# Kernel tuning notes

Measured on AMD Instinct MI355X. Metric: run time of the kernel, lower is better.

Reference implementation:

```python
import jax, jax.numpy as jnp
import numpy as np

N, E1, E2, P, H = 4096, 131072, 131072, 65536, 128
ROLE_VOCAB, ROLE_DIM, IDX_VOCAB, IDX_DIM = 8, 16, 1024, 8


def _lin_init(key, fan_in, fan_out):
    k1, k2 = jax.random.split(key)
    bound = 1.0 / np.sqrt(fan_in)
    W = jax.random.uniform(k1, (fan_in, fan_out), jnp.float32, -bound, bound)
    b = jax.random.uniform(k2, (fan_out,), jnp.float32, -bound, bound)
    return W, b


def setup_inputs() -> dict:
    key = jax.random.key(0)
    ks = jax.random.split(key, 24)
    d = {}
    d["block_features"] = jax.random.normal(ks[0], (N, 16), jnp.float32)
    d["role_ids"] = jax.random.randint(ks[1], (N,), 0, ROLE_VOCAB)
    d["b2b_src"] = jax.random.randint(ks[2], (E1,), 0, N)
    d["b2b_dst"] = jax.random.randint(ks[3], (E1,), 0, N)
    d["b2b_w"] = jax.random.uniform(ks[4], (E1,), jnp.float32)
    d["p2b_pin"] = jax.random.randint(ks[5], (E2,), 0, P)
    d["p2b_block"] = jax.random.randint(ks[6], (E2,), 0, N)
    d["p2b_w"] = jax.random.uniform(ks[7], (E2,), jnp.float32)
    d["pins_pos"] = jax.random.normal(ks[8], (P, 2), jnp.float32)
    d["area_targets"] = jax.random.uniform(ks[9], (N,), jnp.float32)
    # parameters
    d["role_emb"] = jax.random.normal(ks[10], (ROLE_VOCAB, ROLE_DIM), jnp.float32)
    d["idx_emb"] = jax.random.normal(ks[11], (IDX_VOCAB, IDX_DIM), jnp.float32)
    d["in_W1"], d["in_b1"] = _lin_init(ks[12], 16 + IDX_DIM + ROLE_DIM, H)
    d["in_W2"], d["in_b2"] = _lin_init(ks[13], H, H)
    d["b2b_W1"], d["b2b_b1"] = _lin_init(ks[14], 2 * H + 1, H)
    d["b2b_W2"], d["b2b_b2"] = _lin_init(ks[15], H, H)
    d["p2b_W1"], d["p2b_b1"] = _lin_init(ks[16], H + 3, H)
    d["p2b_W2"], d["p2b_b2"] = _lin_init(ks[17], H, H)
    d["self_W"], d["self_b"] = _lin_init(ks[18], H, H)
    d["ln_g"] = jnp.ones((H,), jnp.float32)
    d["ln_b"] = jnp.zeros((H,), jnp.float32)
    d["gp_W1"], d["gp_b1"] = _lin_init(ks[19], 2 * H, H)
    d["gp_W2"], d["gp_b2"] = _lin_init(ks[20], H, H)
    return d


def _mlp2(x, W1, b1, W2, b2):
    return jax.nn.relu(x @ W1 + b1) @ W2 + b2


def _forward(block_features, role_ids, b2b_src, b2b_dst, b2b_w, p2b_pin, p2b_block,
             p2b_w, pins_pos, area_targets, role_emb, idx_emb, in_W1, in_b1, in_W2,
             in_b2, b2b_W1, b2b_b1, b2b_W2, b2b_b2, p2b_W1, p2b_b1, p2b_W2, p2b_b2,
             self_W, self_b, ln_g, ln_b, gp_W1, gp_b1, gp_W2, gp_b2):
    n = block_features.shape[0]
    role_e = role_emb[role_ids]                       # [N, role_dim]
    idx_e = idx_emb[jnp.arange(n) % IDX_VOCAB]        # [N, idx_dim]
    x = jnp.concatenate([block_features, role_e, idx_e], axis=-1)
    h = jax.nn.relu(_mlp2(x, in_W1, in_b1, in_W2, in_b2))  # input_proj ends in ReLU

    # --- b2b messages: two directed messages per undirected edge ---
    max_b2b = jax.lax.stop_gradient(jnp.maximum(jnp.max(jnp.abs(b2b_w)), 1.0))
    w = (b2b_w / max_b2b)[:, None]                    # [E1, 1]
    hi, hj = h[b2b_src], h[b2b_dst]                   # [E1, H]
    m_ij = _mlp2(jnp.concatenate([hi, hj, w], -1), b2b_W1, b2b_b1, b2b_W2, b2b_b2)
    m_ji = _mlp2(jnp.concatenate([hj, hi, w], -1), b2b_W1, b2b_b1, b2b_W2, b2b_b2)
    agg = jnp.zeros_like(h).at[b2b_src].add(m_ij).at[b2b_dst].add(m_ji)

    # --- p2b messages ---
    total_area = jnp.maximum(jnp.sum(area_targets), 1e-6)
    case_scale = jax.lax.stop_gradient(jnp.maximum(jnp.sqrt(total_area), 1e-6))
    max_p2b = jax.lax.stop_gradient(jnp.maximum(jnp.max(jnp.abs(p2b_w)), 1.0))
    pin_feats = jnp.concatenate(
        [pins_pos[p2b_pin] / case_scale, (p2b_w / max_p2b)[:, None]], axis=-1)  # [E2, 3]
    m_p = _mlp2(jnp.concatenate([h[p2b_block], pin_feats], -1),
                p2b_W1, p2b_b1, p2b_W2, p2b_b2)
    agg = agg.at[p2b_block].add(m_p)

    # --- combine + LayerNorm ---
    z = h @ self_W + self_b + agg
    mu = jnp.mean(z, axis=-1, keepdims=True)
    var = jnp.mean(jnp.square(z - mu), axis=-1, keepdims=True)
    block_embeddings = (z - mu) / jnp.sqrt(var + 1e-5) * ln_g + ln_b

    pooled = jnp.concatenate(
        [block_embeddings.mean(axis=0), block_embeddings.max(axis=0)], axis=-1)
    graph_embedding = _mlp2(pooled, gp_W1, gp_b1, gp_W2, gp_b2)
    return block_embeddings, graph_embedding


def reference(block_features, role_ids, b2b_src, b2b_dst, b2b_w, p2b_pin, p2b_block,
              p2b_w, pins_pos, area_targets, role_emb, idx_emb, in_W1, in_b1, in_W2,
              in_b2, b2b_W1, b2b_b1, b2b_W2, b2b_b2, p2b_W1, p2b_b1, p2b_W2, p2b_b2,
              self_W, self_b, ln_g, ln_b, gp_W1, gp_b1, gp_W2, gp_b2):
    block_embeddings, graph_embedding = _forward(
        block_features, role_ids, b2b_src, b2b_dst, b2b_w, p2b_pin, p2b_block,
        p2b_w, pins_pos, area_targets, role_emb, idx_emb, in_W1, in_b1, in_W2,
        in_b2, b2b_W1, b2b_b1, b2b_W2, b2b_b2, p2b_W1, p2b_b1, p2b_W2, p2b_b2,
        self_W, self_b, ln_g, ln_b, gp_W1, gp_b1, gp_W2, gp_b2)
    block_mask = jnp.ones((block_features.shape[0],), dtype=bool)
    return block_embeddings, graph_embedding, block_mask
```

## Files before the change

kernel.cpp:

```cpp
#include <hip/hip_runtime.h>
#include <hip/hip_bf16.h>

#define N_NODES 4096
#define HDIM    128
#define E1      131072
#define E2      131072
#define NMSG_B2B (2 * E1)
#define CAPB    192
#define CAPP    96

#define OFF_PSUM   8
#define OFF_PMAX   136
#define OFF_HB     264
#define OFF_P      (OFF_HB + 262144)
#define OFF_Q      (OFF_P + 524288)
#define OFF_R      (OFF_Q + 524288)
#define OFF_CP     (OFF_R + 524288)
#define OFF_B2H    (OFF_CP + 24576)
#define OFF_B2L    (OFF_B2H + 8192)
#define OFF_P2H    (OFF_B2L + 8192)
#define OFF_P2L    (OFF_P2H + 8192)
#define OFF_SWP    (OFF_P2L + 8192)
#define OFF_IW1    (OFF_SWP + 8192)
#define OFF_IW2    (OFF_IW1 + 4096)
#define OFF_WLAST  (OFF_IW2 + 8192)
#define OFF_PEXTRA (OFF_WLAST + 128)
#define OFF_CNTB   (OFF_PEXTRA + 384)
#define OFF_CNTP   (OFF_CNTB + 4096)
#define OFF_BKB    (OFF_CNTP + 4096)
#define OFF_BKP    (OFF_BKB + 2 * N_NODES * CAPB)
#define WS_FLOATS  (OFF_BKP + 2 * N_NODES * CAPP)

typedef short short8 __attribute__((ext_vector_type(8)));
typedef float f32x4 __attribute__((ext_vector_type(4)));

__device__ __forceinline__ unsigned short f2bf(float f) {
  union { float f; unsigned u; } v; v.f = f;
  unsigned r = v.u + 0x7fffu + ((v.u >> 16) & 1u);
  return (unsigned short)(r >> 16);
}
__device__ __forceinline__ float bf2f(unsigned short h) {
  return __uint_as_float((unsigned)h << 16);
}
__device__ __forceinline__ int il(int c) { return ((c & 63) << 1) | (c >> 6); }

__global__ __launch_bounds__(256) void setup_kernel(const float* __restrict__ b2bw,
                                                    const float* __restrict__ p2bw,
                                                    const float* __restrict__ area,
                                                    const float* __restrict__ bW1,
                                                    const float* __restrict__ bW2,
                                                    const float* __restrict__ pW1,
                                                    const float* __restrict__ pW2,
                                                    const float* __restrict__ sWm,
                                                    const float* __restrict__ iW1,
                                                    const float* __restrict__ iW2,
                                                    float* __restrict__ ws) {
  __shared__ float red[256];
  int b = blockIdx.x, t = threadIdx.x;
  if (b < 32) {
    float m = 0.f;
    for (int i = b * 256 + t; i < E1; i += 32 * 256) m = fmaxf(m, fabsf(b2bw[i]));
    red[t] = m; __syncthreads();
    for (int s = 128; s > 0; s >>= 1) { if (t < s) red[t] = fmaxf(red[t], red[t + s]); __syncthreads(); }
    if (t == 0) atomicMax((unsigned*)&ws[0], __float_as_uint(red[0]));
  } else if (b < 64) {
    float m = 0.f;
    for (int i = (b - 32) * 256 + t; i < E2; i += 32 * 256) m = fmaxf(m, fabsf(p2bw[i]));
    red[t] = m; __syncthreads();
    for (int s = 128; s > 0; s >>= 1) { if (t < s) red[t] = fmaxf(red[t], red[t + s]); __syncthreads(); }
    if (t == 0) atomicMax((unsigned*)&ws[1], __float_as_uint(red[0]));
  } else if (b < 96) {
    float s0 = 0.f;
    for (int i = (b - 64) * 256 + t; i < N_NODES; i += 32 * 256) s0 += area[i];
    red[t] = s0; __syncthreads();
    for (int s = 128; s > 0; s >>= 1) { if (t < s) red[t] += red[t + s]; __syncthreads(); }
    if (t == 0) atomicAdd(&ws[2], red[0]);
  } else if (b == 96) {
    if (t < HDIM) ((int*)ws)[OFF_PMAX + t] = 0x80000000;
  } else {
    unsigned short* Cp  = (unsigned short*)(ws + OFF_CP);
    unsigned short* B2h = (unsigned short*)(ws + OFF_B2H);
    unsigned short* B2l = (unsigned short*)(ws + OFF_B2L);
    unsigned short* P2h = (unsigned short*)(ws + OFF_P2H);
    unsigned short* P2l = (unsigned short*)(ws + OFF_P2L);
    unsigned short* Swp = (unsigned short*)(ws + OFF_SWP);
    unsigned short* I1p = (unsigned short*)(ws + OFF_IW1);
    unsigned short* I2p = (unsigned short*)(ws + OFF_IW2);
    float* wlast = ws + OFF_WLAST;
    float* pextra = ws + OFF_PEXTRA;
    const int total = 156160;
    for (int x = (b - 97) * 256 + t; x < total; x += 128 * 256) {
      if (x < 49152) {
        int j = x & 7, lane = (x >> 3) & 63, ks = (x >> 9) & 3, nc = x >> 11;
        int col = nc * 16 + (lane & 15), k = ks * 32 + (lane >> 4) * 8 + j;
        float v;
        if (col < 128)      v = bW1[k * 128 + col];
        else if (col < 256) v = bW1[(128 + k) * 128 + (col - 128)];
        else                v = pW1[k * 128 + (col - 256)];
        Cp[x] = f2bf(v);
      } else if (x < 114688) {
        int u = (x - 49152) & 16383, which = (x - 49152) >> 14;
        int j = u & 7, lane = (u >> 3) & 63, ks = (u >> 9) & 3, nt = u >> 11;
        int n = nt * 16 + (lane & 15), k = ks * 32 + (lane >> 4) * 8 + j;
        float v = (which < 2) ? bW2[k * 128 + n] : pW2[k * 128 + n];
        unsigned short hi = f2bf(v);
        unsigned short outv = (which & 1) ? f2bf(v - bf2f(hi)) : hi;
        ((which < 2) ? ((which & 1) ? B2l : B2h) : ((which & 1) ? P2l : P2h))[u] = outv;
      } else if (x < 131072) {
        int u = x - 114688;
        int j = u & 7, lane = (u >> 3) & 63, ks = (u >> 9) & 3, nt = u >> 11;
        int n = nt * 16 + (lane & 15), k = ks * 32 + (lane >> 4) * 8 + j;
        Swp[u] = f2bf(sWm[k * 128 + n]);
      } else if (x < 139264) {
        int u = x - 131072;
        int j = u & 7, lane = (u >> 3) & 63, ks = (u >> 9) & 1, nt = u >> 10;
        int n = nt * 16 + (lane & 15), k = ks * 32 + (lane >> 4) * 8 + j;
        I1p[u] = (k < 40) ? f2bf(iW1[k * 128 + n]) : 0;
      } else if (x < 155648) {
        int u = x - 139264;
        int j = u & 7, lane = (u >> 3) & 63, ks = (u >> 9) & 3, nt = u >> 11;
        int n = nt * 16 + (lane & 15), k = ks * 32 + (lane >> 4) * 8 + j;
        I2p[u] = f2bf(iW2[k * 128 + n]);
      } else if (x < 155776) {
        int c = x - 155648;
        wlast[il(c)] = bW1[256 * 128 + c];
      } else {
        int u = x - 155776;
        int r = u >> 7, c = u & 127;
        pextra[r * 128 + il(c)] = pW1[(128 + r) * 128 + c];
      }
    }
  }
}

__global__ __launch_bounds__(512) void mid_kernel(const int* __restrict__ src,
                                                  const int* __restrict__ dst,
                                                  const int* __restrict__ pblk,
                                                  const int* __restrict__ ppin,
                                                  const float* __restrict__ bwv,
                                                  const float* __restrict__ pwv,
                                                  const float* __restrict__ pins,
                                                  const float* __restrict__ bfeat,
                                                  const int* __restrict__ rid,
                                                  const float* __restrict__ remb,
                                                  const float* __restrict__ iemb,
                                                  const float* __restrict__ ib1,
                                                  const float* __restrict__ ib2,
                                                  const float* __restrict__ bb1,
                                                  const float* __restrict__ pb1,
                                                  float* __restrict__ ws,
                                                  unsigned short* __restrict__ hb) {
  __shared__ __attribute__((aligned(16))) unsigned short xs[16 * 72];
  __shared__ __attribute__((aligned(16))) unsigned short h1s[16 * 136];
  __shared__ __attribute__((aligned(16))) unsigned short hs[16 * 136];
  int tid = threadIdx.x;
  if (blockIdx.x < 768) {
    int i = blockIdx.x * 512 + tid;
    int* cntB = (int*)ws + OFF_CNTB;
    int* cntP = (int*)ws + OFF_CNTP;
    uint2* BKB = (uint2*)((int*)ws + OFF_BKB);
    uint2* BKP = (uint2*)((int*)ws + OFF_BKP);
    if (i < NMSG_B2B) {
      int e = i >> 1, d = i & 1;
      int tg = d ? dst[e] : src[e];
      int o  = d ? src[e] : dst[e];
      int pos = atomicAdd(&cntB[tg], 1);
      if (pos < CAPB) {
        uint2 v; v.x = (unsigned)o; v.y = __float_as_uint(bwv[e]);
        BKB[tg * CAPB + pos] = v;
      }
    } else {
      int e = i - NMSG_B2B;
      int pin = ppin[e];
      int tg = pblk[e];
      int pos = atomicAdd(&cntP[tg], 1);
      if (pos < CAPP) {
        uint2 v;
        v.x = ((unsigned)f2bf(pins[pin * 2 + 1]) << 16) | (unsigned)f2bf(pins[pin * 2]);
        v.y = __float_as_uint(pwv[e]);
        BKP[tg * CAPP + pos] = v;
      }
    }
    return;
  }
  const unsigned short* I1p = (const unsigned short*)(ws + OFF_IW1);
  const unsigned short* I2p = (const unsigned short*)(ws + OFF_IW2);
  const unsigned short* Cp  = (const unsigned short*)(ws + OFF_CP);
  float* P = ws + OFF_P;
  float* Q = ws + OFF_Q;
  float* R = ws + OFF_R;
  int n0 = (blockIdx.x - 768) * 16;
  for (int idx = tid; idx < 1024; idx += 512) {
    int m = idx >> 6, c = idx & 63;
    int n = n0 + m;
    float v = 0.f;
    if (c < 16)      v = bfeat[n * 16 + c];
    else if (c < 32) v = remb[rid[n] * 16 + (c - 16)];
    else if (c < 40) v = iemb[(n & 1023) * 8 + (c - 32)];
    xs[m * 72 + c] = f2bf(v);
  }
  __syncthreads();
  int lane = tid & 63, wv = tid >> 6;
  int l15 = lane & 15, q = lane >> 4;
  f32x4 zero = {0.f, 0.f, 0.f, 0.f};
  f32x4 a1 = zero;
#pragma unroll
  for (int ks = 0; ks < 2; ks++) {
    short8 af = *(const short8*)(&xs[l15 * 72 + ks * 32 + q * 8]);
    short8 bfr = *(const short8*)(I1p + ((wv * 2 + ks) * 64 + lane) * 8);
    a1 = __builtin_amdgcn_mfma_f32_16x16x32_bf16(af, bfr, a1, 0, 0, 0);
  }
  {
    int n = wv * 16 + l15;
    float b = ib1[n];
#pragma unroll
    for (int r = 0; r < 4; r++)
      h1s[(q * 4 + r) * 136 + n] = f2bf(fmaxf(a1[r] + b, 0.f));
  }
  __syncthreads();
  f32x4 a2 = zero;
#pragma unroll
  for (int ks = 0; ks < 4; ks++) {
    short8 af = *(const short8*)(&h1s[l15 * 136 + ks * 32 + q * 8]);
    short8 bfr = *(const short8*)(I2p + ((wv * 4 + ks) * 64 + lane) * 8);
    a2 = __builtin_amdgcn_mfma_f32_16x16x32_bf16(af, bfr, a2, 0, 0, 0);
  }
  {
    int n = wv * 16 + l15;
    float b = ib2[n];
#pragma unroll
    for (int r = 0; r < 4; r++) {
      unsigned short hv = f2bf(fmaxf(a2[r] + b, 0.f));
      hs[(q * 4 + r) * 136 + n] = hv;
      hb[(n0 + q * 4 + r) * 128 + n] = hv;
    }
  }
  __syncthreads();
  f32x4 a3[3];
#pragma unroll
  for (int i = 0; i < 3; i++) a3[i] = zero;
#pragma unroll
  for (int ks = 0; ks < 4; ks++) {
    short8 af = *(const short8*)(&hs[l15 * 136 + ks * 32 + q * 8]);
#pragma unroll
    for (int j = 0; j < 3; j++) {
      short8 bfr = *(const short8*)(Cp + (((3 * wv + j) * 4 + ks) * 64 + lane) * 8);
      a3[j] = __builtin_amdgcn_mfma_f32_16x16x32_bf16(af, bfr, a3[j], 0, 0, 0);
    }
  }
#pragma unroll
  for (int j = 0; j < 3; j++) {
    int col = (3 * wv + j) * 16 + l15;
    int arr = col >> 7, cc = col & 127;
    float bias = (arr == 0) ? bb1[cc] : ((arr == 2) ? pb1[cc] : 0.f);
    float* dstp = (arr == 0) ? P : ((arr == 1) ? Q : R);
    int ic = il(cc);
#pragma unroll
    for (int r = 0; r < 4; r++)
      dstp[(n0 + q * 4 + r) * 128 + ic] = a3[j][r] + bias;
  }
}

__global__ __launch_bounds__(1024) void fused_kernel(const unsigned short* __restrict__ hb,
                                                     const float* __restrict__ sb,
                                                     const float* __restrict__ lng,
                                                     const float* __restrict__ lnb,
                                                     const float* __restrict__ bb2,
                                                     const float* __restrict__ pb2,
                                                     const float* __restrict__ gW1,
                                                     const float* __restrict__ gb1,
                                                     const float* __restrict__ gW2,
                                                     const float* __restrict__ gb2,
                                                     float* __restrict__ ws,
                                                     float* __restrict__ out) {
  __shared__ __attribute__((aligned(16))) unsigned short A[16 * 648];
  __shared__ float zp[2][16 * 128];
  __shared__ float zs[16 * 133];
  __shared__ float muS[16], rsg[16];
  __shared__ float partS[16][16], partQ[16][16];
  __shared__ float psumL[8][128];
  __shared__ int   pmaxL[8][128];
  __shared__ int   isLast;
  int tid = threadIdx.x;
  int n0 = blockIdx.x * 16;
  int lane = tid & 63, wv = tid >> 6;
  if (tid < 256) {
    int m = tid >> 4, o = (tid & 15) * 8;
    *(uint4*)(&A[m * 648 + o]) = *(const uint4*)(hb + (n0 + m) * 128 + o);
  }
  {
    const int* cntB = (const int*)ws + OFF_CNTB;
    const int* cntP = (const int*)ws + OFF_CNTP;
    const uint2* BKB = (const uint2*)((const int*)ws + OFF_BKB);
    const uint2* BKP = (const uint2*)((const int*)ws + OFF_BKP);
    const float* Pm = ws + OFF_P;
    const float* Qm = ws + OFF_Q;
    const float* Rm = ws + OFF_R;
    float invb = 1.f / fmaxf(__uint_as_float(((const unsigned*)ws)[0]), 1.f);
    float invp = 1.f / fmaxf(__uint_as_float(((const unsigned*)ws)[1]), 1.f);
    float cs = fmaxf(sqrtf(fmaxf(ws[2], 1e-6f)), 1e-6f);
    float invc = 1.f / cs;
    float2 wlr = *(const float2*)(ws + OFF_WLAST + 2 * lane);
    float2 e0r = *(const float2*)(ws + OFF_PEXTRA + 2 * lane);
    float2 e1r = *(const float2*)(ws + OFF_PEXTRA + 128 + 2 * lane);
    float2 e2r = *(const float2*)(ws + OFF_PEXTRA + 256 + 2 * lane);
    float2 wl = {invb * wlr.x, invb * wlr.y};
    float2 e0 = {invc * e0r.x, invc * e0r.y};
    float2 e1 = {invc * e1r.x, invc * e1r.y};
    float2 e2 = {invp * e2r.x, invp * e2r.y};
    int ln = wv;
    int node = n0 + ln;
    {
      int cnt = min(cntB[node], CAPB);
      const uint2* bk = BKB + node * CAPB;
      float2 p = *(const float2*)(Pm + node * 128 + 2 * lane);
      float a0 = 0.f, a1 = 0.f, b0 = 0.f, b1 = 0.f;
      int m = 0;
      for (; m + 8 <= cnt; m += 8) {
        uint2 k0 = bk[m],     k1 = bk[m + 1], k2 = bk[m + 2], k3 = bk[m + 3];
        uint2 k4 = bk[m + 4], k5 = bk[m + 5], k6 = bk[m + 6], k7 = bk[m + 7];
        float2 q0 = *(const float2*)(Qm + k0.x * 128 + 2 * lane);
        float2 q1 = *(const float2*)(Qm + k1.x * 128 + 2 * lane);
        float2 q2 = *(const float2*)(Qm + k2.x * 128 + 2 * lane);
        float2 q3 = *(const float2*)(Qm + k3.x * 128 + 2 * lane);
        float2 q4 = *(const float2*)(Qm + k4.x * 128 + 2 * lane);
        float2 q5 = *(const float2*)(Qm + k5.x * 128 + 2 * lane);
        float2 q6 = *(const float2*)(Qm + k6.x * 128 + 2 * lane);
        float2 q7 = *(const float2*)(Qm + k7.x * 128 + 2 * lane);
        float w0 = __uint_as_float(k0.y), w1 = __uint_as_float(k1.y);
        float w2 = __uint_as_float(k2.y), w3 = __uint_as_float(k3.y);
        float w4 = __uint_as_float(k4.y), w5 = __uint_as_float(k5.y);
        float w6 = __uint_as_float(k6.y), w7 = __uint_as_float(k7.y);
        a0 += fmaxf(fmaf(w0, wl.x, p.x) + q0.x, 0.f);
        a1 += fmaxf(fmaf(w0, wl.y, p.y) + q0.y, 0.f);
        b0 += fmaxf(fmaf(w1, wl.x, p.x) + q1.x, 0.f);
        b1 += fmaxf(fmaf(w1, wl.y, p.y) + q1.y, 0.f);
        a0 += fmaxf(fmaf(w2, wl.x, p.x) + q2.x, 0.f);
        a1 += fmaxf(fmaf(w2, wl.y, p.y) + q2.y, 0.f);
        b0 += fmaxf(fmaf(w3, wl.x, p.x) + q3.x, 0.f);
        b1 += fmaxf(fmaf(w3, wl.y, p.y) + q3.y, 0.f);
        a0 += fmaxf(fmaf(w4, wl.x, p.x) + q4.x, 0.f);
        a1 += fmaxf(fmaf(w4, wl.y, p.y) + q4.y, 0.f);
        b0 += fmaxf(fmaf(w5, wl.x, p.x) + q5.x, 0.f);
        b1 += fmaxf(fmaf(w5, wl.y, p.y) + q5.y, 0.f);
        a0 += fmaxf(fmaf(w6, wl.x, p.x) + q6.x, 0.f);
        a1 += fmaxf(fmaf(w6, wl.y, p.y) + q6.y, 0.f);
        b0 += fmaxf(fmaf(w7, wl.x, p.x) + q7.x, 0.f);
        b1 += fmaxf(fmaf(w7, wl.y, p.y) + q7.y, 0.f);
      }
      for (; m < cnt; m++) {
        uint2 k0 = bk[m];
        float w0 = __uint_as_float(k0.y);
        float2 q0 = *(const float2*)(Qm + k0.x * 128 + 2 * lane);
        a0 += fmaxf(fmaf(w0, wl.x, p.x) + q0.x, 0.f);
        a1 += fmaxf(fmaf(w0, wl.y, p.y) + q0.y, 0.f);
      }
      float s0 = a0 + b0;
      float s1 = a1 + b1;
      unsigned short h0 = f2bf(s0);
      A[ln * 648 + 128 + lane] = h0;
      A[ln * 648 + 256 + lane] = f2bf(s0 - bf2f(h0));
      unsigned short h1v = f2bf(s1);
      A[ln * 648 + 128 + 64 + lane] = h1v;
      A[ln * 648 + 256 + 64 + lane] = f2bf(s1 - bf2f(h1v));
    }
    {
      int cnt = min(cntP[node], CAPP);
      const uint2* bk = BKP + node * CAPP;
      float2 r = *(const float2*)(Rm + node * 128 + 2 * lane);
      float a0 = 0.f, a1 = 0.f, b0 = 0.f, b1 = 0.f;
      int m = 0;
      for (; m + 4 <= cnt; m += 4) {
        uint2 k0 = bk[m], k1 = bk[m + 1], k2 = bk[m + 2], k3 = bk[m + 3];
        float x00 = __uint_as_float((k0.x & 0xFFFFu) << 16);
        float x01 = __uint_as_float(k0.x & 0xFFFF0000u);
        float x02 = __uint_as_float(k0.y);
        float x10 = __uint_as_float((k1.x & 0xFFFFu) << 16);
        float x11 = __uint_as_float(k1.x & 0xFFFF0000u);
        float x12 = __uint_as_float(k1.y);
        float x20 = __uint_as_float((k2.x & 0xFFFFu) << 16);
        float x21 = __uint_as_float(k2.x & 0xFFFF0000u);
        float x22 = __uint_as_float(k2.y);
        float x30 = __uint_as_float((k3.x & 0xFFFFu) << 16);
        float x31 = __uint_as_float(k3.x & 0xFFFF0000u);
        float x32 = __uint_as_float(k3.y);
        a0 += fmaxf(fmaf(x02, e2.x, fmaf(x01, e1.x, fmaf(x00, e0.x, r.x))), 0.f);
        a1 += fmaxf(fmaf(x02, e2.y, fmaf(x01, e1.y, fmaf(x00, e0.y, r.y))), 0.f);
        b0 += fmaxf(fmaf(x12, e2.x, fmaf(x11, e1.x, fmaf(x10, e0.x, r.x))), 0.f);
        b1 += fmaxf(fmaf(x12, e2.y, fmaf(x11, e1.y, fmaf(x10, e0.y, r.y))), 0.f);
        a0 += fmaxf(fmaf(x22, e2.x, fmaf(x21, e1.x, fmaf(x20, e0.x, r.x))), 0.f);
        a1 += fmaxf(fmaf(x22, e2.y, fmaf(x21, e1.y, fmaf(x20, e0.y, r.y))), 0.f);
        b0 += fmaxf(fmaf(x32, e2.x, fmaf(x31, e1.x, fmaf(x30, e0.x, r.x))), 0.f);
        b1 += fmaxf(fmaf(x32, e2.y, fmaf(x31, e1.y, fmaf(x30, e0.y, r.y))), 0.f);
      }
      for (; m < cnt; m++) {
        uint2 k0 = bk[m];
        float x00 = __uint_as_float((k0.x & 0xFFFFu) << 16);
        float x01 = __uint_as_float(k0.x & 0xFFFF0000u);
        float x02 = __uint_as_float(k0.y);
        a0 += fmaxf(fmaf(x02, e2.x, fmaf(x01, e1.x, fmaf(x00, e0.x, r.x))), 0.f);
        a1 += fmaxf(fmaf(x02, e2.y, fmaf(x01, e1.y, fmaf(x00, e0.y, r.y))), 0.f);
      }
      float s0 = a0 + b0;
      float s1 = a1 + b1;
      unsigned short h0 = f2bf(s0);
      A[ln * 648 + 384 + lane] = h0;
      A[ln * 648 + 512 + lane] = f2bf(s0 - bf2f(h0));
      unsigned short h1v = f2bf(s1);
      A[ln * 648 + 384 + 64 + lane] = h1v;
      A[ln * 648 + 512 + 64 + lane] = f2bf(s1 - bf2f(h1v));
    }
  }
  __syncthreads();
  int l15 = lane & 15, q = lane >> 4;
  int ct = wv & 7, half = wv >> 3;
  f32x4 zero = {0.f, 0.f, 0.f, 0.f};
  f32x4 acc = zero;
  const unsigned short* bufs[7] = {
    (const unsigned short*)(ws + OFF_SWP), (const unsigned short*)(ws + OFF_B2H),
    (const unsigned short*)(ws + OFF_B2L), (const unsigned short*)(ws + OFF_B2H),
    (const unsigned short*)(ws + OFF_P2H), (const unsigned short*)(ws + OFF_P2L),
    (const unsigned short*)(ws + OFF_P2H)};
  const int segs[7] = {0, 128, 128, 256, 384, 384, 512};
  int p0 = half ? 4 : 0, p1 = half ? 7 : 4;
  for (int p = p0; p < p1; p++) {
#pragma unroll
    for (int ks = 0; ks < 4; ks++) {
      short8 af = *(const short8*)(&A[l15 * 648 + segs[p] + ks * 32 + q * 8]);
      short8 bfr = *(const short8*)(bufs[p] + ((ct * 4 + ks) * 64 + lane) * 8);
      acc = __builtin_amdgcn_mfma_f32_16x16x32_bf16(af, bfr, acc, 0, 0, 0);
    }
  }
  {
    int nn = ct * 16 + l15;
#pragma unroll
    for (int r = 0; r < 4; r++)
      zp[half][(q * 4 + r) * 128 + nn] = acc[r];
  }
  __syncthreads();
  const int* cntB = (const int*)ws + OFF_CNTB;
  const int* cntP = (const int*)ws + OFF_CNTP;
  {
    int idx = tid;
    for (int rep = 0; rep < 2; rep++, idx += 1024) {
      int row = idx >> 7, c = idx & 127;
      float cb = (float)cntB[n0 + row], cp = (float)cntP[n0 + row];
      zs[row * 133 + c] = zp[0][row * 128 + c] + zp[1][row * 128 + c]
                        + sb[c] + cb * bb2[c] + cp * pb2[c];
    }
  }
  __syncthreads();
  if (tid < 256) {
    int r = tid >> 4, g = tid & 15;
    const float* zr = &zs[r * 133 + g * 8];
    float s = 0.f, s2 = 0.f;
#pragma unroll
    for (int i = 0; i < 8; i++) { float v = zr[i]; s += v; s2 += v * v; }
    partS[r][g] = s; partQ[r][g] = s2;
  }
  __syncthreads();
  if (tid < 16) {
    float s = 0.f, s2 = 0.f;
#pragma unroll
    for (int g = 0; g < 16; g++) { s += partS[tid][g]; s2 += partQ[tid][g]; }
    float m = s * (1.f / 128.f);
    float var = s2 * (1.f / 128.f) - m * m;
    muS[tid] = m;
    rsg[tid] = rsqrtf(fmaxf(var, 0.f) + 1e-5f);
  }
  __syncthreads();
  {
    int c = tid & 127, grp = tid >> 7;
    float g = lng[c], b = lnb[c];
    float ls = 0.f; int lm = 0x80000000;
    for (int r = grp * 2; r < grp * 2 + 2; r++) {
      float v = (zs[r * 133 + c] - muS[r]) * rsg[r] * g + b;
      out[(n0 + r) * 128 + c] = v;
      ls += v;
      int e = __float_as_int(v);
      e = e >= 0 ? e : (e ^ 0x7fffffff);
      lm = max(lm, e);
    }
    psumL[grp][c] = ls; pmaxL[grp][c] = lm;
  }
  __syncthreads();
  if (tid < 128) {
    float s = 0.f; int mx = 0x80000000;
#pragma unroll
    for (int g = 0; g < 8; g++) { s += psumL[g][tid]; mx = max(mx, pmaxL[g][tid]); }
    atomicAdd(&ws[OFF_PSUM + tid], s);
    atomicMax(&((int*)ws)[OFF_PMAX + tid], mx);
  }
  if (tid < 16) out[N_NODES * HDIM + HDIM + n0 + tid] = 1.0f;
  __syncthreads();
  if (tid == 0) {
    __threadfence();
    int v = atomicAdd(&((int*)ws)[3], 1);
    isLast = (v == (int)gridDim.x - 1);
  }
  __syncthreads();
  if (!isLast) return;
  __shared__ float pooled[256];
  __shared__ float gpart[8][128];
  __shared__ float g1[128];
  if (tid < 128) {
    pooled[tid] = atomicAdd(&ws[OFF_PSUM + tid], 0.f) * (1.f / (float)N_NODES);
  } else if (tid < 256) {
    int e = atomicAdd(&((int*)ws)[OFF_PMAX + (tid - 128)], 0);
    int bits = e >= 0 ? e : (e ^ 0x7fffffff);
    pooled[tid] = __int_as_float(bits);
  }
  __syncthreads();
  {
    int c = tid & 127, g = tid >> 7;
    float acc2 = 0.f;
#pragma unroll 8
    for (int k = g * 32; k < g * 32 + 32; k++) acc2 += pooled[k] * gW1[k * 128 + c];
    gpart[g][c] = acc2;
  }
  __syncthreads();
  if (tid < 128) {
    float s = gb1[tid];
#pragma unroll
    for (int g = 0; g < 8; g++) s += gpart[g][tid];
    g1[tid] = fmaxf(s, 0.f);
  }
  __syncthreads();
  {
    int c = tid & 127, g = tid >> 7;
    float acc2 = 0.f;
#pragma unroll 8
    for (int k = g * 16; k < g * 16 + 16; k++) acc2 += g1[k] * gW2[k * 128 + c];
    gpart[g][c] = acc2;
  }
  __syncthreads();
  if (tid < 128) {
    float s = gb2[tid];
#pragma unroll
    for (int g = 0; g < 8; g++) s += gpart[g][tid];
    out[N_NODES * HDIM + tid] = s;
  }
}

extern "C" void kernel_launch(void* const* d_in, const int* in_sizes, int n_in,
                              void* d_out, int out_size, void* d_ws, size_t ws_size,
                              hipStream_t stream) {
  const float* bfeat = (const float*)d_in[0];
  const int*   rid   = (const int*)d_in[1];
  const int*   bsrc  = (const int*)d_in[2];
  const int*   bdst  = (const int*)d_in[3];
  const float* bw    = (const float*)d_in[4];
  const int*   ppin  = (const int*)d_in[5];
  const int*   pblk  = (const int*)d_in[6];
  const float* pw    = (const float*)d_in[7];
  const float* pins  = (const float*)d_in[8];
  const float* area  = (const float*)d_in[9];
  const float* remb  = (const float*)d_in[10];
  const float* iemb  = (const float*)d_in[11];
  const float* inW1  = (const float*)d_in[12];
  const float* inb1  = (const float*)d_in[13];
  const float* inW2  = (const float*)d_in[14];
  const float* inb2  = (const float*)d_in[15];
  const float* bW1   = (const float*)d_in[16];
  const float* bb1   = (const float*)d_in[17];
  const float* bW2   = (const float*)d_in[18];
  const float* bb2   = (const float*)d_in[19];
  const float* pW1   = (const float*)d_in[20];
  const float* pb1   = (const float*)d_in[21];
  const float* pW2   = (const float*)d_in[22];
  const float* pb2   = (const float*)d_in[23];
  const float* sW    = (const float*)d_in[24];
  const float* sb    = (const float*)d_in[25];
  const float* lng   = (const float*)d_in[26];
  const float* lnb   = (const float*)d_in[27];
  const float* gW1   = (const float*)d_in[28];
  const float* gb1   = (const float*)d_in[29];
  const float* gW2   = (const float*)d_in[30];
  const float* gb2   = (const float*)d_in[31];

  float* ws  = (float*)d_ws;
  float* out = (float*)d_out;
  unsigned short* hb = (unsigned short*)(ws + OFF_HB);
  int* cntB = (int*)ws + OFF_CNTB;

  hipMemsetAsync(d_ws, 0, 264 * sizeof(float), stream);
  hipMemsetAsync((void*)cntB, 0, 2 * 4096 * sizeof(int), stream);
  setup_kernel<<<225, 256, 0, stream>>>(bw, pw, area,
                                        bW1, bW2, pW1, pW2, sW, inW1, inW2, ws);
  mid_kernel<<<1024, 512, 0, stream>>>(bsrc, bdst, pblk, ppin, bw, pw, pins,
                                       bfeat, rid, remb, iemb, inb1, inb2, bb1, pb1,
                                       ws, hb);
  fused_kernel<<<256, 1024, 0, stream>>>(hb, sb, lng, lnb, bb2, pb2,
                                         gW1, gb1, gW2, gb2, ws, out);
}
```

Measured before the change: 196.0 us.

## Move edge bucketing into setup kernel and widen node kernel to 1024 threads

```diff
diff --git a/kernel.cpp b/kernel.cpp
--- a/kernel.cpp
+++ b/kernel.cpp
@@ -47,6 +47,11 @@
 __global__ __launch_bounds__(256) void setup_kernel(const float* __restrict__ b2bw,
                                                     const float* __restrict__ p2bw,
                                                     const float* __restrict__ area,
+                                                    const int* __restrict__ src,
+                                                    const int* __restrict__ dst,
+                                                    const int* __restrict__ pblk,
+                                                    const int* __restrict__ ppin,
+                                                    const float* __restrict__ pins,
                                                     const float* __restrict__ bW1,
                                                     const float* __restrict__ bW2,
                                                     const float* __restrict__ pW1,
@@ -77,6 +82,33 @@
     if (t == 0) atomicAdd(&ws[2], red[0]);
   } else if (b == 96) {
     if (t < HDIM) ((int*)ws)[OFF_PMAX + t] = 0x80000000;
+  } else if (b < 1633) {
+    int i = (b - 97) * 256 + t;
+    int* cntB = (int*)ws + OFF_CNTB;
+    int* cntP = (int*)ws + OFF_CNTP;
+    uint2* BKB = (uint2*)((int*)ws + OFF_BKB);
+    uint2* BKP = (uint2*)((int*)ws + OFF_BKP);
+    if (i < NMSG_B2B) {
+      int e = i >> 1, d = i & 1;
+      int tg = d ? dst[e] : src[e];
+      int o  = d ? src[e] : dst[e];
+      int pos = atomicAdd(&cntB[tg], 1);
+      if (pos < CAPB) {
+        uint2 v; v.x = (unsigned)o; v.y = __float_as_uint(b2bw[e]);
+        BKB[tg * CAPB + pos] = v;
+      }
+    } else if (i < NMSG_B2B + E2) {
+      int e = i - NMSG_B2B;
+      int pin = ppin[e];
+      int tg = pblk[e];
+      int pos = atomicAdd(&cntP[tg], 1);
+      if (pos < CAPP) {
+        uint2 v;
+        v.x = ((unsigned)f2bf(pins[pin * 2 + 1]) << 16) | (unsigned)f2bf(pins[pin * 2]);
+        v.y = __float_as_uint(p2bw[e]);
+        BKP[tg * CAPP + pos] = v;
+      }
+    }
   } else {
     unsigned short* Cp  = (unsigned short*)(ws + OFF_CP);
     unsigned short* B2h = (unsigned short*)(ws + OFF_B2H);
@@ -89,7 +121,7 @@
     float* wlast = ws + OFF_WLAST;
     float* pextra = ws + OFF_PEXTRA;
     const int total = 156160;
-    for (int x = (b - 97) * 256 + t; x < total; x += 128 * 256) {
+    for (int x = (b - 1633) * 256 + t; x < total; x += 128 * 256) {
       if (x < 49152) {
         int j = x & 7, lane = (x >> 3) & 63, ks = (x >> 9) & 3, nc = x >> 11;
         int col = nc * 16 + (lane & 15), k = ks * 32 + (lane >> 4) * 8 + j;
@@ -133,65 +165,29 @@
   }
 }
 
-__global__ __launch_bounds__(512) void mid_kernel(const int* __restrict__ src,
-                                                  const int* __restrict__ dst,
-                                                  const int* __restrict__ pblk,
-                                                  const int* __restrict__ ppin,
-                                                  const float* __restrict__ bwv,
-                                                  const float* __restrict__ pwv,
-                                                  const float* __restrict__ pins,
-                                                  const float* __restrict__ bfeat,
-                                                  const int* __restrict__ rid,
-                                                  const float* __restrict__ remb,
-                                                  const float* __restrict__ iemb,
-                                                  const float* __restrict__ ib1,
-                                                  const float* __restrict__ ib2,
-                                                  const float* __restrict__ bb1,
-                                                  const float* __restrict__ pb1,
-                                                  float* __restrict__ ws,
-                                                  unsigned short* __restrict__ hb) {
+__global__ __launch_bounds__(1024) void node_kernel(const float* __restrict__ bfeat,
+                                                    const int* __restrict__ rid,
+                                                    const float* __restrict__ remb,
+                                                    const float* __restrict__ iemb,
+                                                    const float* __restrict__ ib1,
+                                                    const float* __restrict__ ib2,
+                                                    const float* __restrict__ bb1,
+                                                    const float* __restrict__ pb1,
+                                                    float* __restrict__ ws,
+                                                    unsigned short* __restrict__ hb) {
   __shared__ __attribute__((aligned(16))) unsigned short xs[16 * 72];
   __shared__ __attribute__((aligned(16))) unsigned short h1s[16 * 136];
   __shared__ __attribute__((aligned(16))) unsigned short hs[16 * 136];
   int tid = threadIdx.x;
-  if (blockIdx.x < 768) {
-    int i = blockIdx.x * 512 + tid;
-    int* cntB = (int*)ws + OFF_CNTB;
-    int* cntP = (int*)ws + OFF_CNTP;
-    uint2* BKB = (uint2*)((int*)ws + OFF_BKB);
-    uint2* BKP = (uint2*)((int*)ws + OFF_BKP);
-    if (i < NMSG_B2B) {
-      int e = i >> 1, d = i & 1;
-      int tg = d ? dst[e] : src[e];
-      int o  = d ? src[e] : dst[e];
-      int pos = atomicAdd(&cntB[tg], 1);
-      if (pos < CAPB) {
-        uint2 v; v.x = (unsigned)o; v.y = __float_as_uint(bwv[e]);
-        BKB[tg * CAPB + pos] = v;
-      }
-    } else {
-      int e = i - NMSG_B2B;
-      int pin = ppin[e];
-      int tg = pblk[e];
-      int pos = atomicAdd(&cntP[tg], 1);
-      if (pos < CAPP) {
-        uint2 v;
-        v.x = ((unsigned)f2bf(pins[pin * 2 + 1]) << 16) | (unsigned)f2bf(pins[pin * 2]);
-        v.y = __float_as_uint(pwv[e]);
-        BKP[tg * CAPP + pos] = v;
-      }
-    }
-    return;
-  }
   const unsigned short* I1p = (const unsigned short*)(ws + OFF_IW1);
   const unsigned short* I2p = (const unsigned short*)(ws + OFF_IW2);
   const unsigned short* Cp  = (const unsigned short*)(ws + OFF_CP);
   float* P = ws + OFF_P;
   float* Q = ws + OFF_Q;
   float* R = ws + OFF_R;
-  int n0 = (blockIdx.x - 768) * 16;
-  for (int idx = tid; idx < 1024; idx += 512) {
-    int m = idx >> 6, c = idx & 63;
+  int n0 = blockIdx.x * 16;
+  if (tid < 1024) {
+    int m = tid >> 6, c = tid & 63;
     int n = n0 + m;
     float v = 0.f;
     if (c < 16)      v = bfeat[n * 16 + c];
@@ -203,14 +199,14 @@
   int lane = tid & 63, wv = tid >> 6;
   int l15 = lane & 15, q = lane >> 4;
   f32x4 zero = {0.f, 0.f, 0.f, 0.f};
-  f32x4 a1 = zero;
-#pragma unroll
-  for (int ks = 0; ks < 2; ks++) {
-    short8 af = *(const short8*)(&xs[l15 * 72 + ks * 32 + q * 8]);
-    short8 bfr = *(const short8*)(I1p + ((wv * 2 + ks) * 64 + lane) * 8);
-    a1 = __builtin_amdgcn_mfma_f32_16x16x32_bf16(af, bfr, a1, 0, 0, 0);
-  }
-  {
+  if (wv < 8) {
+    f32x4 a1 = zero;
+#pragma unroll
+    for (int ks = 0; ks < 2; ks++) {
+      short8 af = *(const short8*)(&xs[l15 * 72 + ks * 32 + q * 8]);
+      short8 bfr = *(const short8*)(I1p + ((wv * 2 + ks) * 64 + lane) * 8);
+      a1 = __builtin_amdgcn_mfma_f32_16x16x32_bf16(af, bfr, a1, 0, 0, 0);
+    }
     int n = wv * 16 + l15;
     float b = ib1[n];
 #pragma unroll
@@ -218,14 +214,14 @@
       h1s[(q * 4 + r) * 136 + n] = f2bf(fmaxf(a1[r] + b, 0.f));
   }
   __syncthreads();
-  f32x4 a2 = zero;
-#pragma unroll
-  for (int ks = 0; ks < 4; ks++) {
-    short8 af = *(const short8*)(&h1s[l15 * 136 + ks * 32 + q * 8]);
-    short8 bfr = *(const short8*)(I2p + ((wv * 4 + ks) * 64 + lane) * 8);
-    a2 = __builtin_amdgcn_mfma_f32_16x16x32_bf16(af, bfr, a2, 0, 0, 0);
-  }
-  {
+  if (wv < 8) {
+    f32x4 a2 = zero;
+#pragma unroll
+    for (int ks = 0; ks < 4; ks++) {
+      short8 af = *(const short8*)(&h1s[l15 * 136 + ks * 32 + q * 8]);
+      short8 bfr = *(const short8*)(I2p + ((wv * 4 + ks) * 64 + lane) * 8);
+      a2 = __builtin_amdgcn_mfma_f32_16x16x32_bf16(af, bfr, a2, 0, 0, 0);
+    }
     int n = wv * 16 + l15;
     float b = ib2[n];
 #pragma unroll
@@ -236,21 +232,24 @@
     }
   }
   __syncthreads();
-  f32x4 a3[3];
-#pragma unroll
-  for (int i = 0; i < 3; i++) a3[i] = zero;
+  int tiles[2];
+  tiles[0] = wv;
+  tiles[1] = (wv < 8) ? (16 + wv) : -1;
+  f32x4 a3[2]; a3[0] = zero; a3[1] = zero;
 #pragma unroll
   for (int ks = 0; ks < 4; ks++) {
     short8 af = *(const short8*)(&hs[l15 * 136 + ks * 32 + q * 8]);
 #pragma unroll
-    for (int j = 0; j < 3; j++) {
-      short8 bfr = *(const short8*)(Cp + (((3 * wv + j) * 4 + ks) * 64 + lane) * 8);
+    for (int j = 0; j < 2; j++) {
+      if (tiles[j] < 0) continue;
+      short8 bfr = *(const short8*)(Cp + ((tiles[j] * 4 + ks) * 64 + lane) * 8);
       a3[j] = __builtin_amdgcn_mfma_f32_16x16x32_bf16(af, bfr, a3[j], 0, 0, 0);
     }
   }
 #pragma unroll
-  for (int j = 0; j < 3; j++) {
-    int col = (3 * wv + j) * 16 + l15;
+  for (int j = 0; j < 2; j++) {
+    if (tiles[j] < 0) continue;
+    int col = tiles[j] * 16 + l15;
     int arr = col >> 7, cc = col & 127;
     float bias = (arr == 0) ? bb1[cc] : ((arr == 2) ? pb1[cc] : 0.f);
     float* dstp = (arr == 0) ? P : ((arr == 1) ? Q : R);
@@ -511,7 +510,7 @@
     pooled[tid] = __int_as_float(bits);
   }
   __syncthreads();
-  {
+  if (tid < 1024) {
     int c = tid & 127, g = tid >> 7;
     float acc2 = 0.f;
 #pragma unroll 8
@@ -526,7 +525,7 @@
     g1[tid] = fmaxf(s, 0.f);
   }
   __syncthreads();
-  {
+  if (tid < 1024) {
     int c = tid & 127, g = tid >> 7;
     float acc2 = 0.f;
 #pragma unroll 8
@@ -585,11 +584,10 @@
 
   hipMemsetAsync(d_ws, 0, 264 * sizeof(float), stream);
   hipMemsetAsync((void*)cntB, 0, 2 * 4096 * sizeof(int), stream);
-  setup_kernel<<<225, 256, 0, stream>>>(bw, pw, area,
-                                        bW1, bW2, pW1, pW2, sW, inW1, inW2, ws);
-  mid_kernel<<<1024, 512, 0, stream>>>(bsrc, bdst, pblk, ppin, bw, pw, pins,
-                                       bfeat, rid, remb, iemb, inb1, inb2, bb1, pb1,
-                                       ws, hb);
+  setup_kernel<<<1761, 256, 0, stream>>>(bw, pw, area, bsrc, bdst, pblk, ppin, pins,
+                                         bW1, bW2, pW1, pW2, sW, inW1, inW2, ws);
+  node_kernel<<<N_NODES / 16, 1024, 0, stream>>>(bfeat, rid, remb, iemb,
+                                                 inb1, inb2, bb1, pb1, ws, hb);
   fused_kernel<<<256, 1024, 0, stream>>>(hb, sb, lng, lnb, bb2, pb2,
                                          gW1, gb1, gW2, gb2, ws, out);
 }
```

Result: no change. 198.6 us (+1.3%).
